# Optimization experiments

Measured on AMD Instinct MI355X. Metric: run time of the kernel, lower is better.

Reference implementation:

```python
import jax, jax.numpy as jnp
import numpy as np

NUM_LAYERS = 16
IN_SIZE = 1024
OUT_SIZE = 1024
B, S = 64, 128

def setup_inputs() -> dict:
    key = jax.random.key(0)
    k1, k2, k3 = jax.random.split(key, 3)
    x = jax.random.normal(k1, (B, S, IN_SIZE), dtype=jnp.float32)
    layer_idx = jax.random.randint(k2, (S,), 0, NUM_LAYERS)
    weight = jax.random.normal(k3, (NUM_LAYERS, OUT_SIZE, IN_SIZE), dtype=jnp.float32)
    return {"x": x, "layer_idx": layer_idx, "weight": weight}

def reference(x, layer_idx, weight):
    # Branch: layer_idx is 1D with len == S (per-position weight selection).
    # Gather per-position weights [S, O, D] and do one batched contraction,
    # equivalent to the Python loop of per-step matmuls in the original.
    w = weight[layer_idx]                       # [S, O, D]
    out = jnp.einsum('bsd,sod->bso', x, w)      # [B, S, O]
    return out
```

## Files before the change

kernel.cpp:

```cpp
#include <hip/hip_runtime.h>
#include <hip/hip_bf16.h>

#define B_ 64
#define S_ 128
#define D_ 1024
#define O_ 1024
#define L_ 16

typedef __bf16 bf16x8 __attribute__((ext_vector_type(8)));
typedef float f32x4 __attribute__((ext_vector_type(4)));
typedef unsigned u32x4 __attribute__((ext_vector_type(4)));

#define WS_W   0ull
#define WS_X   33554432ull
#define WS_P   50331648ull
#define WS_NEED (50331664ull + 72ull * 16ull)

__device__ __forceinline__ unsigned f2bf2(float a, float b) {
    union { float f; unsigned u; } x{a}, y{b};
    unsigned lo = x.u + 0x7FFFu + ((x.u >> 16) & 1u);
    unsigned hi = y.u + 0x7FFFu + ((y.u >> 16) & 1u);
    return (lo >> 16) | (hi & 0xFFFF0000u);
}

__device__ __forceinline__ void gload16(const void* g, void* l) {
    __builtin_amdgcn_global_load_lds(
        (const __attribute__((address_space(1))) void*)g,
        (__attribute__((address_space(3))) void*)l, 16, 0, 0);
}

__global__ __launch_bounds__(256) void moshi_convert(
    const float* __restrict__ x, const float* __restrict__ w,
    const int* __restrict__ lidx, unsigned char* __restrict__ ws) {
    if (blockIdx.x == 0 && threadIdx.x < 16) {
        int t = threadIdx.x;
        int cnt[16];
        #pragma unroll 1
        for (int m = 0; m < 16; ++m) cnt[m] = 0;
        for (int s = 0; s < S_; ++s) ++cnt[lidx[s]];
        int off = 0;
        for (int m = 0; m < t; ++m) off += (cnt[m] + 1) >> 1;
        int4* pairs = (int4*)(ws + WS_P + 16);
        int k = 0, prev = -1;
        for (int s = 0; s < S_; ++s) {
            if (lidx[s] == t) {
                if (k & 1) pairs[off + (k >> 1)] = make_int4(prev, s, t, 0);
                prev = s; ++k;
            }
        }
        if (k & 1) pairs[off + (k >> 1)] = make_int4(prev, prev, t, 0);
        if (t == 0) {
            int tot = 0;
            for (int m = 0; m < 16; ++m) tot += (cnt[m] + 1) >> 1;
            *(int*)(ws + WS_P) = tot;
        }
    }
    const int TW4 = L_ * O_ * D_ / 16;
    const int t0 = blockIdx.x * 256 + threadIdx.x;
    if (t0 < TW4) {
        const float4* src = reinterpret_cast<const float4*>(w) + 4ull * t0;
        float4 v0 = src[0], v1 = src[1], v2 = src[2], v3 = src[3];
        u32x4 lo = { f2bf2(v0.x, v0.y), f2bf2(v0.z, v0.w),
                     f2bf2(v1.x, v1.y), f2bf2(v1.z, v1.w) };
        u32x4 hi = { f2bf2(v2.x, v2.y), f2bf2(v2.z, v2.w),
                     f2bf2(v3.x, v3.y), f2bf2(v3.z, v3.w) };
        int f = t0 * 4;
        int d4 = f & 255, o = (f >> 8) & 1023, l = f >> 18;
        int nt = o >> 7, row = o & 127, kt = d4 >> 4;
        unsigned base = ((unsigned)((l * 8 + nt) * 16 + kt)) * 16384u + (unsigned)(row * 128);
        unsigned c = (unsigned)((d4 & 15) * 8);
        unsigned k = (unsigned)((row & 7) << 4);
        *reinterpret_cast<u32x4*>(ws + WS_W + base + (c ^ k))        = lo;
        *reinterpret_cast<u32x4*>(ws + WS_W + base + ((c + 16) ^ k)) = hi;
    } else {
        int g = (t0 - TW4) * 4;
        const float4* src = reinterpret_cast<const float4*>(x) + 4ull * (t0 - TW4);
        float4 v0 = src[0], v1 = src[1], v2 = src[2], v3 = src[3];
        u32x4 lo = { f2bf2(v0.x, v0.y), f2bf2(v0.z, v0.w),
                     f2bf2(v1.x, v1.y), f2bf2(v1.z, v1.w) };
        u32x4 hi = { f2bf2(v2.x, v2.y), f2bf2(v2.z, v2.w),
                     f2bf2(v3.x, v3.y), f2bf2(v3.z, v3.w) };
        int d4 = g & 255, s = (g >> 8) & 127, b = g >> 15;
        int kt = d4 >> 4;
        unsigned base = ((unsigned)(s * 16 + kt)) * 8192u + (unsigned)(b * 128);
        unsigned c = (unsigned)((d4 & 15) * 8);
        unsigned k = (unsigned)((b & 7) << 4);
        *reinterpret_cast<u32x4*>(ws + WS_X + base + (c ^ k))        = lo;
        *reinterpret_cast<u32x4*>(ws + WS_X + base + ((c + 16) ^ k)) = hi;
    }
}

__global__ __launch_bounds__(512) void moshi_gemm_n128(
    const unsigned char* __restrict__ ws, float* __restrict__ out) {
    __shared__ __align__(16) unsigned char lw[16384];
    __shared__ __align__(16) unsigned char lx[16384];

    const int bid = (blockIdx.x & 7) * 72 + (blockIdx.x >> 3);
    const int pi = bid >> 3;
    const int nt = bid & 7;
    const int np = *reinterpret_cast<const int*>(ws + WS_P);
    if (pi >= np) return;
    const int4 pr = *reinterpret_cast<const int4*>(ws + WS_P + 16 + 16ull * pi);
    const int s0 = pr.x, s1 = pr.y, l = pr.z;

    const unsigned char* wt  = ws + WS_W + ((size_t)(l * 8 + nt) * 16) * 16384;
    const unsigned char* xt0 = ws + WS_X + (size_t)s0 * 16 * 8192;
    const unsigned char* xt1 = ws + WS_X + (size_t)s1 * 16 * 8192;

    const int tid = threadIdx.x, lane = tid & 63, wid = tid >> 6;
    const int wm = wid >> 2, wn = wid & 3;
    const int swz = (lane & 7) << 4;
    const int kb  = (lane >> 4) << 4;
    const int a_base = (wm * 64 + (lane & 15)) * 128 + kb;
    const int b_base = (wn * 32 + (lane & 15)) * 128 + kb;

    f32x4 acc[4][2];
    #pragma unroll
    for (int i = 0; i < 4; ++i)
        #pragma unroll
        for (int j = 0; j < 2; ++j) acc[i][j] = (f32x4)0.0f;

    #pragma unroll 1
    for (int kt = 0; kt < 16; ++kt) {
        __syncthreads();
        gload16(wt  + (size_t)kt * 16384 + tid * 16,        lw + tid * 16);
        gload16(wt  + (size_t)kt * 16384 + tid * 16 + 8192, lw + tid * 16 + 8192);
        gload16(xt0 + (size_t)kt * 8192  + tid * 16,        lx + tid * 16);
        gload16(xt1 + (size_t)kt * 8192  + tid * 16,        lx + tid * 16 + 8192);
        __syncthreads();
        #pragma unroll
        for (int kk = 0; kk < 2; ++kk) {
            bf16x8 af[4], bfr[2];
            #pragma unroll
            for (int mi = 0; mi < 4; ++mi)
                af[mi] = *reinterpret_cast<const bf16x8*>(
                    lx + (((a_base + kk * 64) ^ swz) + mi * 2048));
            #pragma unroll
            for (int ni = 0; ni < 2; ++ni)
                bfr[ni] = *reinterpret_cast<const bf16x8*>(
                    lw + (((b_base + kk * 64) ^ swz) + ni * 2048));
            #pragma unroll
            for (int mi = 0; mi < 4; ++mi)
                #pragma unroll
                for (int ni = 0; ni < 2; ++ni)
                    acc[mi][ni] = __builtin_amdgcn_mfma_f32_16x16x32_bf16(
                        af[mi], bfr[ni], acc[mi][ni], 0, 0, 0);
        }
    }

    const int s_sel = wm ? s1 : s0;
    const int col0 = nt * 128 + wn * 32 + (lane & 15);
    const int r0 = (lane >> 4) << 2;
    #pragma unroll
    for (int mi = 0; mi < 4; ++mi)
        #pragma unroll
        for (int ni = 0; ni < 2; ++ni)
            #pragma unroll
            for (int r = 0; r < 4; ++r) {
                int b = mi * 16 + r0 + r;
                out[((size_t)b * S_ + s_sel) * O_ + col0 + ni * 16] = acc[mi][ni][r];
            }
}

__global__ __launch_bounds__(256) void moshi_flin_fallback(
    const float* __restrict__ x, const int* __restrict__ lidx,
    const float* __restrict__ w, float* __restrict__ out) {
    __shared__ __align__(16) unsigned char lxs[64 * 128];
    __shared__ __align__(16) unsigned char lws[128 * 128];
    const int bid = blockIdx.x;
    const int s = bid >> 3, n0 = (bid & 7) << 7;
    const int tid = threadIdx.x, lane = tid & 63, wid = tid >> 6;
    const int idx = lidx[s];
    const float* wb = w + (size_t)idx * O_ * D_ + (size_t)n0 * D_;
    const float* xb = x + (size_t)s * D_;
    const int swz = (lane & 7) << 4;
    const int kb = (lane >> 4) << 4;
    const int a_base = (lane & 15) * 128 + kb;
    const int b_base = (wid * 32 + (lane & 15)) * 128 + kb;
    f32x4 acc[4][2];
    #pragma unroll
    for (int i = 0; i < 4; ++i)
        #pragma unroll
        for (int j = 0; j < 2; ++j) acc[i][j] = (f32x4)0.0f;
    for (int kt = 0; kt < D_; kt += 64) {
        __syncthreads();
        #pragma unroll
        for (int p = 0; p < 4; ++p) {
            int f = tid + p * 256, row = f >> 4, cc = (f & 15) << 2;
            const float4 v = *reinterpret_cast<const float4*>(
                xb + (size_t)row * (S_ * D_) + kt + cc);
            uint2 pk = { f2bf2(v.x, v.y), f2bf2(v.z, v.w) };
            *reinterpret_cast<uint2*>(&lxs[(row * 128 + cc * 2) ^ ((row & 7) << 4)]) = pk;
        }
        #pragma unroll
        for (int p = 0; p < 8; ++p) {
            int f = tid + p * 256, row = f >> 4, cc = (f & 15) << 2;
            const float4 v = *reinterpret_cast<const float4*>(
                wb + (size_t)row * D_ + kt + cc);
            uint2 pk = { f2bf2(v.x, v.y), f2bf2(v.z, v.w) };
            *reinterpret_cast<uint2*>(&lws[(row * 128 + cc * 2) ^ ((row & 7) << 4)]) = pk;
        }
        __syncthreads();
        #pragma unroll
        for (int kk = 0; kk < 2; ++kk) {
            bf16x8 af[4], bfr[2];
            #pragma unroll
            for (int mi = 0; mi < 4; ++mi)
                af[mi] = *reinterpret_cast<const bf16x8*>(
                    &lxs[(((a_base + kk * 64) ^ swz) + mi * 2048)]);
            #pragma unroll
            for (int ni = 0; ni < 2; ++ni)
                bfr[ni] = *reinterpret_cast<const bf16x8*>(
                    &lws[(((b_base + kk * 64) ^ swz) + ni * 2048)]);
            #pragma unroll
            for (int mi = 0; mi < 4; ++mi)
                #pragma unroll
                for (int ni = 0; ni < 2; ++ni)
                    acc[mi][ni] = __builtin_amdgcn_mfma_f32_16x16x32_bf16(
                        af[mi], bfr[ni], acc[mi][ni], 0, 0, 0);
        }
    }
    float* ob = out + (size_t)s * O_ + n0 + wid * 32 + (lane & 15);
    const int r0 = (lane >> 4) << 2;
    #pragma unroll
    for (int mi = 0; mi < 4; ++mi)
        #pragma unroll
        for (int ni = 0; ni < 2; ++ni)
            #pragma unroll
            for (int r = 0; r < 4; ++r) {
                int b = mi * 16 + r0 + r;
                ob[(size_t)b * (S_ * O_) + ni * 16] = acc[mi][ni][r];
            }
}

extern "C" void kernel_launch(void* const* d_in, const int* in_sizes, int n_in,
                              void* d_out, int out_size, void* d_ws, size_t ws_size,
                              hipStream_t stream) {
    const float* x  = (const float*)d_in[0];
    const int* lidx = (const int*)d_in[1];
    const float* w  = (const float*)d_in[2];
    float* out      = (float*)d_out;

    if (ws_size < WS_NEED) {
        moshi_flin_fallback<<<dim3(128 * 8), dim3(256), 0, stream>>>(x, lidx, w, out);
        return;
    }
    unsigned char* ws = (unsigned char*)d_ws;
    moshi_convert<<<dim3(6144), dim3(256), 0, stream>>>(x, w, lidx, ws);
    moshi_gemm_n128<<<dim3(72 * 8), dim3(512), 0, stream>>>(ws, out);
}
```

Measured before the change: 58.91 us.

## Convert to plain row-major bf16 and apply LDS swizzle in GEMM loads

The conversion kernel drops its tiled, swizzled output layout and writes plain row-major bf16 copies of weight and x, using simple coalesced 8-byte stores. The GEMM kernel now computes the XOR swizzle on the global source address, so each thread fetches a 16-byte chunk from a 2 KB-strided row instead of a contiguous tile. The aim is to make the bandwidth-bound conversion pass cheaper, in exchange for less contiguous global reads during the GEMM. It also adds a minimum-blocks occupancy hint to the GEMM's launch bounds.

```diff
diff --git a/kernel.cpp b/kernel.cpp
--- a/kernel.cpp
+++ b/kernel.cpp
@@ -9,7 +9,6 @@
 
 typedef __bf16 bf16x8 __attribute__((ext_vector_type(8)));
 typedef float f32x4 __attribute__((ext_vector_type(4)));
-typedef unsigned u32x4 __attribute__((ext_vector_type(4)));
 
 #define WS_W   0ull
 #define WS_X   33554432ull
@@ -55,42 +54,24 @@
             *(int*)(ws + WS_P) = tot;
         }
     }
-    const int TW4 = L_ * O_ * D_ / 16;
-    const int t0 = blockIdx.x * 256 + threadIdx.x;
-    if (t0 < TW4) {
-        const float4* src = reinterpret_cast<const float4*>(w) + 4ull * t0;
-        float4 v0 = src[0], v1 = src[1], v2 = src[2], v3 = src[3];
-        u32x4 lo = { f2bf2(v0.x, v0.y), f2bf2(v0.z, v0.w),
-                     f2bf2(v1.x, v1.y), f2bf2(v1.z, v1.w) };
-        u32x4 hi = { f2bf2(v2.x, v2.y), f2bf2(v2.z, v2.w),
-                     f2bf2(v3.x, v3.y), f2bf2(v3.z, v3.w) };
-        int f = t0 * 4;
-        int d4 = f & 255, o = (f >> 8) & 1023, l = f >> 18;
-        int nt = o >> 7, row = o & 127, kt = d4 >> 4;
-        unsigned base = ((unsigned)((l * 8 + nt) * 16 + kt)) * 16384u + (unsigned)(row * 128);
-        unsigned c = (unsigned)((d4 & 15) * 8);
-        unsigned k = (unsigned)((row & 7) << 4);
-        *reinterpret_cast<u32x4*>(ws + WS_W + base + (c ^ k))        = lo;
-        *reinterpret_cast<u32x4*>(ws + WS_W + base + ((c + 16) ^ k)) = hi;
+    const float4* src;
+    uint2* dst;
+    unsigned i0 = blockIdx.x * 512 + threadIdx.x;
+    if (blockIdx.x < 8192) {
+        src = reinterpret_cast<const float4*>(w);
+        dst = reinterpret_cast<uint2*>(ws + WS_W);
     } else {
-        int g = (t0 - TW4) * 4;
-        const float4* src = reinterpret_cast<const float4*>(x) + 4ull * (t0 - TW4);
-        float4 v0 = src[0], v1 = src[1], v2 = src[2], v3 = src[3];
-        u32x4 lo = { f2bf2(v0.x, v0.y), f2bf2(v0.z, v0.w),
-                     f2bf2(v1.x, v1.y), f2bf2(v1.z, v1.w) };
-        u32x4 hi = { f2bf2(v2.x, v2.y), f2bf2(v2.z, v2.w),
-                     f2bf2(v3.x, v3.y), f2bf2(v3.z, v3.w) };
-        int d4 = g & 255, s = (g >> 8) & 127, b = g >> 15;
-        int kt = d4 >> 4;
-        unsigned base = ((unsigned)(s * 16 + kt)) * 8192u + (unsigned)(b * 128);
-        unsigned c = (unsigned)((d4 & 15) * 8);
-        unsigned k = (unsigned)((b & 7) << 4);
-        *reinterpret_cast<u32x4*>(ws + WS_X + base + (c ^ k))        = lo;
-        *reinterpret_cast<u32x4*>(ws + WS_X + base + ((c + 16) ^ k)) = hi;
-    }
-}
-
-__global__ __launch_bounds__(512) void moshi_gemm_n128(
+        src = reinterpret_cast<const float4*>(x);
+        dst = reinterpret_cast<uint2*>(ws + WS_X);
+        i0 -= 4194304u;
+    }
+    float4 v0 = src[i0];
+    float4 v1 = src[i0 + 256];
+    dst[i0]       = make_uint2(f2bf2(v0.x, v0.y), f2bf2(v0.z, v0.w));
+    dst[i0 + 256] = make_uint2(f2bf2(v1.x, v1.y), f2bf2(v1.z, v1.w));
+}
+
+__global__ __launch_bounds__(512, 4) void moshi_gemm_n128(
     const unsigned char* __restrict__ ws, float* __restrict__ out) {
     __shared__ __align__(16) unsigned char lw[16384];
     __shared__ __align__(16) unsigned char lx[16384];
@@ -103,11 +84,19 @@
     const int4 pr = *reinterpret_cast<const int4*>(ws + WS_P + 16 + 16ull * pi);
     const int s0 = pr.x, s1 = pr.y, l = pr.z;
 
-    const unsigned char* wt  = ws + WS_W + ((size_t)(l * 8 + nt) * 16) * 16384;
-    const unsigned char* xt0 = ws + WS_X + (size_t)s0 * 16 * 8192;
-    const unsigned char* xt1 = ws + WS_X + (size_t)s1 * 16 * 8192;
-
     const int tid = threadIdx.x, lane = tid & 63, wid = tid >> 6;
+
+    const int rowq = tid >> 3;
+    const int c16  = (tid & 7) << 4;
+    const int csw  = c16 ^ ((rowq & 7) << 4);
+    const unsigned char* wsrc0 = ws + WS_W
+        + ((size_t)(l * 1024 + nt * 128 + rowq) << 11) + csw;
+    const unsigned char* wsrc1 = wsrc0 + ((size_t)64 << 11);
+    const unsigned char* xsrc0 = ws + WS_X
+        + ((size_t)(rowq * 128 + s0) << 11) + csw;
+    const unsigned char* xsrc1 = ws + WS_X
+        + ((size_t)(rowq * 128 + s1) << 11) + csw;
+
     const int wm = wid >> 2, wn = wid & 3;
     const int swz = (lane & 7) << 4;
     const int kb  = (lane >> 4) << 4;
@@ -123,10 +112,10 @@
     #pragma unroll 1
     for (int kt = 0; kt < 16; ++kt) {
         __syncthreads();
-        gload16(wt  + (size_t)kt * 16384 + tid * 16,        lw + tid * 16);
-        gload16(wt  + (size_t)kt * 16384 + tid * 16 + 8192, lw + tid * 16 + 8192);
-        gload16(xt0 + (size_t)kt * 8192  + tid * 16,        lx + tid * 16);
-        gload16(xt1 + (size_t)kt * 8192  + tid * 16,        lx + tid * 16 + 8192);
+        gload16(wsrc0 + kt * 128, lw + tid * 16);
+        gload16(wsrc1 + kt * 128, lw + tid * 16 + 8192);
+        gload16(xsrc0 + kt * 128, lx + tid * 16);
+        gload16(xsrc1 + kt * 128, lx + tid * 16 + 8192);
         __syncthreads();
         #pragma unroll
         for (int kk = 0; kk < 2; ++kk) {
@@ -246,6 +235,6 @@
         return;
     }
     unsigned char* ws = (unsigned char*)d_ws;
-    moshi_convert<<<dim3(6144), dim3(256), 0, stream>>>(x, w, lidx, ws);
+    moshi_convert<<<dim3(12288), dim3(256), 0, stream>>>(x, w, lidx, ws);
     moshi_gemm_n128<<<dim3(72 * 8), dim3(512), 0, stream>>>(ws, out);
 }
```

New measurement: 56.29 us. 4.4% less time.
